# Performance work log

Hardware: AMD Instinct MI355X
Metric: run time of the kernel (lower is better)

## Reference

```python
import jax, jax.numpy as jnp
import numpy as np

B, R, H, W = 128, 8, 256, 256


def _conv(x, w, b):
    # x: [1, C_in, h, w], w: [C_out, C_in, 3, 3]; stride 2, pad 1, then bias + ReLU
    y = jax.lax.conv_general_dilated(
        x, w, window_strides=(2, 2), padding=((1, 1), (1, 1)),
        dimension_numbers=('NCHW', 'OIHW', 'NCHW'))
    return jax.nn.relu(y + b[None, :, None, None])


def _single(x, w1, b1, w2, b2, w3, b3, fw, fb):
    # x: [3, H, W]; one sample through its region's CNN expert
    h = x[None]                      # [1,3,H,W]
    h = _conv(h, w1, b1)             # [1,32,H/2,W/2]
    h = _conv(h, w2, b2)             # [1,64,H/4,W/4]
    h = _conv(h, w3, b3)             # [1,128,H/8,W/8]
    feat = h.mean(axis=(2, 3))[0]    # [128] global average pool
    return fw @ feat + fb            # [num_classes]


def setup_inputs() -> dict:
    key = jax.random.key(0)
    ks = jax.random.split(key, 10)
    s = 0.05
    return {
        'image': jax.random.normal(ks[0], (B, 3, H, W), jnp.float32),
        'region': jax.random.randint(ks[1], (B,), 0, R, jnp.int64),
        'w1': jax.random.normal(ks[2], (R, 32, 3, 3, 3), jnp.float32) * s,
        'b1': jax.random.normal(ks[3], (R, 32), jnp.float32) * s,
        'w2': jax.random.normal(ks[4], (R, 64, 32, 3, 3), jnp.float32) * s,
        'b2': jax.random.normal(ks[5], (R, 64), jnp.float32) * s,
        'w3': jax.random.normal(ks[6], (R, 128, 64, 3, 3), jnp.float32) * s,
        'b3': jax.random.normal(ks[7], (R, 128), jnp.float32) * s,
        'fw': jax.random.normal(ks[8], (R, 2, 128), jnp.float32) * s,
        'fb': jax.random.normal(ks[9], (R, 2), jnp.float32) * s,
    }


def reference(image, region, w1, b1, w2, b2, w3, b3, fw, fb):
    # MoE-style dispatch: gather each sample's region weights, vmap per-sample expert.
    r = region.astype(jnp.int32)
    pw = [jnp.take(p, r, axis=0) for p in (w1, b1, w2, b2, w3, b3, fw, fb)]
    out = jax.vmap(_single)(image, *pw)  # [B, num_classes]
    return out
```

## Files before the change

### kernel.cpp

```cpp
#include <hip/hip_runtime.h>
#include <cstdint>


typedef __attribute__((ext_vector_type(8))) short short8;
typedef __attribute__((ext_vector_type(4))) float floatx4;
typedef __attribute__((ext_vector_type(4))) unsigned short ushort4v;
typedef __attribute__((ext_vector_type(4))) float float4v;

__device__ inline unsigned short f2bf(float f) {
  union { float f; unsigned u; } x;
  x.f = f;
  unsigned u = x.u;
  u += 0x7FFFu + ((u >> 16) & 1u);
  return (unsigned short)(u >> 16);
}

__device__ inline void g2l16(const unsigned short* g, unsigned short* l) {
  __builtin_amdgcn_global_load_lds(
      (const __attribute__((address_space(1))) unsigned int*)g,
      (__attribute__((address_space(3))) unsigned int*)(unsigned int)(uintptr_t)l,
      16, 0, 0);
}

__global__ __launch_bounds__(256) void setup_k(
    const int* __restrict__ rp, int* __restrict__ rout, float* __restrict__ feat,
    const float* __restrict__ w1, unsigned short* __restrict__ w1p,
    const float* __restrict__ w2, unsigned short* __restrict__ w2p,
    const float* __restrict__ w3, unsigned short* __restrict__ w3p,
    unsigned short* __restrict__ h2p, int nhalo) {
  const int tid = threadIdx.x;
  if (blockIdx.x == 0) {
    __shared__ int is64;
    if (tid < 64) {
      int v = rp[2 * tid + 1];
      unsigned long long ball = __ballot(v != 0);
      if (tid == 0) is64 = (ball == 0ULL) ? 1 : 0;
    }
    __syncthreads();
    if (tid < 128) {
      int r = is64 ? rp[2 * tid] : rp[tid];
      rout[tid] = r & 7;
      float* fr = feat + tid * 128;
      for (int j = 0; j < 128; ++j) fr[j] = 0.f;
    }
    return;
  }
  int t = (blockIdx.x - 1) * 256 + tid;
  if (t < 16384) {
    int j = t & 7, lane = (t >> 3) & 63, mt = (t >> 9) & 1, kg = (t >> 10) & 1,
        r = t >> 11;
    int oc = mt * 16 + (lane & 15);
    int q = (lane >> 4) & 3;
    int row = kg * 2 + (q >> 1);
    int idx = (q & 1) * 8 + j;
    int kx = idx >> 2, c = idx & 3;
    float val = 0.f;
    if (row < 3 && kx < 3 && c < 3)
      val = w1[((r * 32 + oc) * 3 + c) * 9 + row * 3 + kx];
    w1p[t] = f2bf(val);
  } else if (t < 163840) {
    int t2 = t - 16384;
    int j = t2 & 7, lane = (t2 >> 3) & 63;
    int u = t2 >> 9;
    int mt = u & 3; u >>= 2;
    int tap = u % 9;
    int r = u / 9;
    int oc = mt * 16 + (lane & 15);
    int ic = ((lane >> 4) & 3) * 8 + j;
    w2p[t2] = f2bf(w2[((r * 64 + oc) * 32 + ic) * 9 + tap]);
  } else if (t < 753664) {
    int t3 = t - 163840;
    int j = t3 & 7, lane = (t3 >> 3) & 63;
    int u = t3 >> 9;
    int mt = u & 7; u >>= 3;
    int s = u & 1; u >>= 1;
    int tap = u % 9;
    int r = u / 9;
    int oc = mt * 16 + (lane & 15);
    int ic = s * 32 + ((lane >> 4) & 3) * 8 + j;
    w3p[t3] = f2bf(w3[((r * 128 + oc) * 64 + ic) * 9 + tap]);
  } else {
    int th = t - 753664;
    if (th < nhalo) {
      int s = th / 260, i = th - s * 260;
      int y, x;
      if (i < 66) { y = 0; x = i; }
      else if (i < 132) { y = 65; x = i - 66; }
      else {
        int ii = i - 132;
        y = 1 + (ii >> 1);
        x = (ii & 1) ? 65 : 0;
      }
      short8 z = {0, 0, 0, 0, 0, 0, 0, 0};
      *(short8*)(h2p + ((size_t)s * 66 * 66 + y * 66 + x) * 8) = z;
    }
  }
}

__global__ __launch_bounds__(256, 3) void conv12_k(
    const float* __restrict__ img, const unsigned short* __restrict__ w1p,
    const float* __restrict__ b1, const unsigned short* __restrict__ w2p,
    const float* __restrict__ b2, const int* __restrict__ rgn,
    unsigned short* __restrict__ outp, int b0) {
  __shared__ unsigned short imgT[11 * 168 * 4];
  __shared__ unsigned short h1T[9 * 4 * 66 * 8];
  __shared__ float sB1[32];
  __shared__ float sB2[64];
  const int tid = threadIdx.x;
  const int xh = blockIdx.x;
  const int oy0 = blockIdx.y * 4;
  const int bl = blockIdx.z;
  const int r = __builtin_amdgcn_readfirstlane(rgn[b0 + bl]);
  if (tid < 32) sB1[tid] = b1[r * 32 + tid];
  if (tid >= 64 && tid < 128) sB2[tid - 64] = b2[r * 64 + (tid - 64)];
  const float* ib = img + (size_t)(b0 + bl) * 3 * 65536;
  const int padx = xh ? 65 : 0;
  const bool skiptop = (oy0 == 0);
  const int rb = xh * 128 - 4;

  const int n = tid & 15, q = (tid >> 4) & 3, wv = tid >> 6;
  const int lane = tid & 63;
  const short8* wpb1 = (const short8*)w1p + (size_t)r * 256 + lane;
  short8 afr1[2][2];
#pragma unroll
  for (int kg = 0; kg < 2; ++kg)
#pragma unroll
    for (int m = 0; m < 2; ++m) afr1[kg][m] = wpb1[(kg * 2 + m) * 64];

  {
    const int nch = 11 * 41;
    for (int seg = 0; seg < nch; seg += 256) {
      int c = seg + tid;
      if (c < nch) {
        int i = c / 41, cq = c - i * 41;
        int rv = 4 * oy0 - 3 + i;
        int cb = rb + 4 * cq;
        unsigned short* dp = &imgT[((size_t)i * 168 + (4 * cq - 1)) * 4];
        if (rv >= 0 && cq > 0 && cb >= 0 && cb + 3 <= 255) {
          const float* p = ib + (size_t)rv * 256 + cb;
          float4v a = *(const float4v*)p;
          float4v bb = *(const float4v*)(p + 65536);
          float4v cc = *(const float4v*)(p + 131072);
#pragma unroll
          for (int e = 0; e < 4; ++e) {
            ushort4v v = {f2bf(a[e]), f2bf(bb[e]), f2bf(cc[e]), 0};
            *(ushort4v*)(dp + e * 4) = v;
          }
        } else {
          for (int e = (cq == 0 ? 1 : 0); e < 4; ++e) {
            int cc2 = cb + e;
            ushort4v v = {0, 0, 0, 0};
            if (rv >= 0 && cc2 >= 0 && cc2 <= 255) {
              const float* p = ib + (size_t)rv * 256 + cc2;
              v.x = f2bf(p[0]);
              v.y = f2bf(p[65536]);
              v.z = f2bf(p[131072]);
            }
            *(ushort4v*)(dp + e * 4) = v;
          }
        }
      }
    }
  }
  {
    short8 z8 = {0, 0, 0, 0, 0, 0, 0, 0};
    if (tid < 36) {
      int hy = tid / 4, cg = tid % 4;
      *(short8*)&h1T[(((size_t)hy * 4 + cg) * 66 + padx) * 8] = z8;
    }
    if (skiptop) {
      for (int c = tid; c < 264; c += 256) {
        int cg = c / 66, x = c - cg * 66;
        *(short8*)&h1T[(((size_t)0 * 4 + cg) * 66 + x) * 8] = z8;
      }
    }
  }

  auto CONV1ROW = [&](int hy, int phaseB) {
    floatx4 a1[5][2];
#pragma unroll
    for (int nt = 0; nt < 5; ++nt)
#pragma unroll
      for (int m = 0; m < 2; ++m) a1[nt][m] = (floatx4){0.f, 0.f, 0.f, 0.f};
#pragma unroll
    for (int kg = 0; kg < 2; ++kg) {
      int row = kg * 2 + (q >> 1);
      int rowc = (row < 3) ? row : 0;
      int tr = 2 * hy + rowc;
      int slot = phaseB ? (tr >= 11 ? tr - 11 : tr) : tr;
#pragma unroll
      for (int nt = 0; nt < 5; ++nt) {
        int lx = nt * 16 + n;
        short8 bfr = *(const short8*)&imgT[((size_t)slot * 168 + 2 * lx) * 4 +
                                           (q & 1) * 8];
#pragma unroll
        for (int m = 0; m < 2; ++m)
          a1[nt][m] = __builtin_amdgcn_mfma_f32_16x16x32_bf16(
              afr1[kg][m], bfr, a1[nt][m], 0, 0, 0);
      }
    }
#pragma unroll
    for (int nt = 0; nt < 5; ++nt) {
      int lx = nt * 16 + n;
      bool ok = (lx <= 65) && (lx != padx) && !(skiptop && hy == 0);
      if (ok) {
#pragma unroll
        for (int m = 0; m < 2; ++m) {
          ushort4v st;
#pragma unroll
          for (int rr = 0; rr < 4; ++rr) {
            float v = a1[nt][m][rr] + sB1[m * 16 + q * 4 + rr];
            st[rr] = f2bf(v > 0.f ? v : 0.f);
          }
          int cg = m * 2 + (q >> 1);
          *(ushort4v*)&h1T[(((size_t)hy * 4 + cg) * 66 + lx) * 8 +
                           (q & 1) * 4] = st;
        }
      }
    }
  };

  __syncthreads();

  float4v Lb0[3], Lb1[3];
  int ok0 = 0, ok1 = 0;
  {
    int c = tid;
    int i = c / 41, cq = c - i * 41;
    int cb = rb + 4 * cq;
    if (cq > 0 && cb >= 0 && cb + 3 <= 255) {
      const float* p = ib + (size_t)(4 * oy0 + 8 + i) * 256 + cb;
      Lb0[0] = *(const float4v*)p;
      Lb0[1] = *(const float4v*)(p + 65536);
      Lb0[2] = *(const float4v*)(p + 131072);
      ok0 = 1;
    }
    c = tid + 256;
    if (c < 328) {
      i = c / 41; cq = c - i * 41; cb = rb + 4 * cq;
      if (cq > 0 && cb >= 0 && cb + 3 <= 255) {
        const float* p = ib + (size_t)(4 * oy0 + 8 + i) * 256 + cb;
        Lb1[0] = *(const float4v*)p;
        Lb1[1] = *(const float4v*)(p + 65536);
        Lb1[2] = *(const float4v*)(p + 131072);
        ok1 = 1;
      }
    }
  }

  for (int hy = wv; hy <= 4; hy += 4) CONV1ROW(hy, 0);
  __syncthreads();

  auto STOREB = [&](int c, const float4v* L, int okf) {
    int i = c / 41, cq = c - i * 41;
    int cb = rb + 4 * cq;
    unsigned short* dp = &imgT[((size_t)i * 168 + (4 * cq - 1)) * 4];
    if (okf) {
#pragma unroll
      for (int e = 0; e < 4; ++e) {
        ushort4v v = {f2bf(L[0][e]), f2bf(L[1][e]), f2bf(L[2][e]), 0};
        *(ushort4v*)(dp + e * 4) = v;
      }
    } else {
      int rv = 4 * oy0 + 8 + i;
      for (int e = (cq == 0 ? 1 : 0); e < 4; ++e) {
        int cc2 = cb + e;
        ushort4v v = {0, 0, 0, 0};
        if (cc2 >= 0 && cc2 <= 255) {
          const float* p = ib + (size_t)rv * 256 + cc2;
          v.x = f2bf(p[0]);
          v.y = f2bf(p[65536]);
          v.z = f2bf(p[131072]);
        }
        *(ushort4v*)(dp + e * 4) = v;
      }
    }
  };
  STOREB(tid, Lb0, ok0);
  if (tid + 256 < 328) STOREB(tid + 256, Lb1, ok1);
  __syncthreads();

  CONV1ROW(5 + wv, 1);
  __syncthreads();

  const short8* wpb2 = (const short8*)w2p + (size_t)r * 9 * 4 * 64 + lane;
  floatx4 a2[2][4];
#pragma unroll
  for (int nt = 0; nt < 2; ++nt)
#pragma unroll
    for (int m = 0; m < 4; ++m) a2[nt][m] = (floatx4){0.f, 0.f, 0.f, 0.f};
#pragma unroll
  for (int tap = 0; tap < 9; ++tap) {
    const int ky = tap / 3, kx = tap % 3;
    short8 af[4];
#pragma unroll
    for (int m = 0; m < 4; ++m) af[m] = wpb2[(tap * 4 + m) * 64];
    short8 bf[2];
#pragma unroll
    for (int nt = 0; nt < 2; ++nt) {
      int ox = nt * 16 + n;
      bf[nt] = *(const short8*)&h1T[((((2 * wv + ky) << 2) + q) * 66 +
                                    (2 * ox + kx)) * 8];
    }
#pragma unroll
    for (int m = 0; m < 4; ++m)
#pragma unroll
      for (int nt = 0; nt < 2; ++nt)
        a2[nt][m] = __builtin_amdgcn_mfma_f32_16x16x32_bf16(af[m], bf[nt],
                                                            a2[nt][m], 0, 0, 0);
  }
  unsigned short* ob = outp + (size_t)bl * 8 * 66 * 66 * 8;
  const int oy = oy0 + wv;
#pragma unroll
  for (int nt = 0; nt < 2; ++nt) {
    int ox = xh * 32 + nt * 16 + n;
#pragma unroll
    for (int m = 0; m < 4; ++m) {
      ushort4v st;
#pragma unroll
      for (int rr = 0; rr < 4; ++rr) {
        float v = a2[nt][m][rr] + sB2[m * 16 + q * 4 + rr];
        st[rr] = f2bf(v > 0.f ? v : 0.f);
      }
      int cg = m * 2 + (q >> 1);
      *(ushort4v*)&ob[(((size_t)cg * 66 + oy + 1) * 66 + ox + 1) * 8 +
                      (q & 1) * 4] = st;
    }
  }
}

__global__ __launch_bounds__(256, 2) void conv3dir2_k(
    const unsigned short* __restrict__ in, const unsigned short* __restrict__ wp,
    const float* __restrict__ bias, const int* __restrict__ rgn,
    float* __restrict__ feat, int b0) {
  __shared__ float sBias[128];
  __shared__ float sGap[4 * 128];
  const int tid = threadIdx.x;
  const int bl = blockIdx.y;
  const int b = b0 + bl;
  const int r = __builtin_amdgcn_readfirstlane(rgn[b]);
  if (tid < 128) sBias[tid] = bias[r * 128 + tid];
  const int oyb = blockIdx.x * 8;
  const unsigned short* gbase = in + (size_t)bl * 8 * 66 * 66 * 8;
  const int lane = tid & 63, wv = tid >> 6;
  const int n = lane & 15, q = (lane >> 4) & 3;
  const short8* wpb = (const short8*)wp + (size_t)r * 9 * 2 * 8 * 64 + lane;

  floatx4 acc[2][2][8];
#pragma unroll
  for (int r2 = 0; r2 < 2; ++r2)
#pragma unroll
    for (int nt = 0; nt < 2; ++nt)
#pragma unroll
      for (int m = 0; m < 8; ++m) acc[r2][nt][m] = (floatx4){0.f, 0.f, 0.f, 0.f};

#pragma unroll
  for (int s = 0; s < 2; ++s) {
    const unsigned short* ab = gbase + (size_t)(s * 4 + q) * 66 * 66 * 8;
#pragma unroll
    for (int tap = 0; tap < 9; ++tap) {
      const int ky = tap / 3, kx = tap % 3;
      short8 bfr[2][2];
#pragma unroll
      for (int r2 = 0; r2 < 2; ++r2)
#pragma unroll
        for (int nt = 0; nt < 2; ++nt) {
          int oy = oyb + 2 * wv + r2;
          int ox = nt * 16 + n;
          bfr[r2][nt] = *(const short8*)&ab[((size_t)(2 * oy + ky) * 66 +
                                             (2 * ox + kx)) * 8];
        }
      short8 afr[8];
#pragma unroll
      for (int m = 0; m < 8; ++m) afr[m] = wpb[((tap * 2 + s) * 8 + m) * 64];
#pragma unroll
      for (int m = 0; m < 8; ++m)
#pragma unroll
        for (int r2 = 0; r2 < 2; ++r2)
#pragma unroll
          for (int nt = 0; nt < 2; ++nt)
            acc[r2][nt][m] = __builtin_amdgcn_mfma_f32_16x16x32_bf16(
                afr[m], bfr[r2][nt], acc[r2][nt][m], 0, 0, 0);
    }
  }

#pragma unroll
  for (int m = 0; m < 8; ++m)
#pragma unroll
    for (int rr = 0; rr < 4; ++rr) {
      float bv = sBias[m * 16 + q * 4 + rr];
      float vs = 0.f;
#pragma unroll
      for (int r2 = 0; r2 < 2; ++r2)
#pragma unroll
        for (int nt = 0; nt < 2; ++nt) {
          float v = acc[r2][nt][m][rr] + bv;
          vs += (v > 0.f ? v : 0.f);
        }
      vs += __shfl_xor(vs, 1, 16);
      vs += __shfl_xor(vs, 2, 16);
      vs += __shfl_xor(vs, 4, 16);
      vs += __shfl_xor(vs, 8, 16);
      if (n == 0) sGap[wv * 128 + m * 16 + q * 4 + rr] = vs;
    }
  __syncthreads();
  if (tid < 128)
    atomicAdd(&feat[b * 128 + tid],
              sGap[tid] + sGap[128 + tid] + sGap[256 + tid] + sGap[384 + tid]);
}

__global__ __launch_bounds__(256) void head_k(
    const float* __restrict__ feat, const float* __restrict__ fw,
    const float* __restrict__ fb, const int* __restrict__ rgn,
    float* __restrict__ out) {
  int t = threadIdx.x;
  int b = t >> 1, c = t & 1;
  int r = rgn[b];
  const float* fwr = fw + (r * 2 + c) * 128;
  const float* fv = feat + b * 128;
  float a = 0.f;
#pragma unroll 8
  for (int j = 0; j < 128; ++j) a = fmaf(fwr[j], fv[j], a);
  out[t] = a * (1.0f / 1024.0f) + fb[r * 2 + c];
}

extern "C" void kernel_launch(void* const* d_in, const int* in_sizes, int n_in,
                              void* d_out, int out_size, void* d_ws, size_t ws_size,
                              hipStream_t stream) {
  const float* img = (const float*)d_in[0];
  const int* rgn_raw = (const int*)d_in[1];
  const float* w1 = (const float*)d_in[2];
  const float* b1 = (const float*)d_in[3];
  const float* w2 = (const float*)d_in[4];
  const float* b2 = (const float*)d_in[5];
  const float* w3 = (const float*)d_in[6];
  const float* b3 = (const float*)d_in[7];
  const float* fw = (const float*)d_in[8];
  const float* fb = (const float*)d_in[9];
  float* out = (float*)d_out;

  const size_t h2p_s = (size_t)8 * 66 * 66 * 8 * 2;

  char* ws = (char*)d_ws;
  size_t off = 0;
  auto alloc = [&](size_t bytes) {
    char* p = ws + off;
    off += (bytes + 255) & ~(size_t)255;
    return p;
  };
  unsigned short* h2p = (unsigned short*)alloc((size_t)128 * h2p_s);
  unsigned short* w1p = (unsigned short*)alloc((size_t)16384 * 2);
  unsigned short* w2p = (unsigned short*)alloc((size_t)147456 * 2);
  unsigned short* w3p = (unsigned short*)alloc((size_t)589824 * 2);
  float* feat = (float*)alloc((size_t)128 * 128 * 4);
  int* rgn = (int*)alloc((size_t)128 * 4);

  {
    int nhalo = 128 * 8 * 260;
    int total = 753664 + nhalo;
    int nblk = 1 + (total + 255) / 256;
    hipLaunchKernelGGL(setup_k, dim3(nblk), dim3(256), 0, stream,
                       rgn_raw, rgn, feat, w1, w1p, w2, w2p, w3, w3p, h2p, nhalo);
  }

  hipLaunchKernelGGL(conv12_k, dim3(2, 16, 128), dim3(256), 0, stream,
                     img, w1p, b1, w2p, b2, rgn, h2p, 0);
  hipLaunchKernelGGL(conv3dir2_k, dim3(4, 128), dim3(256), 0, stream,
                     h2p, w3p, b3, rgn, feat, 0);
  hipLaunchKernelGGL(head_k, dim3(1), dim3(256), 0, stream, feat, fw, fb, rgn, out);
}
```

Measured before the change: 284.3 us.

## Halve conv1+conv2 row tile, drop two-phase image staging, vectorize head dot product

The fused conv1/conv2 kernel now produces 2 output rows per block instead of 4, so the grid doubles. The h1 LDS buffer shrinks, the occupancy hint rises from 3 to 4 blocks, and the second-phase image prefetch and register staging are removed. Each wave now computes one 16-pixel conv2 tile and loads weights per tap inside the loop. The price is more redundant conv1 halo rows and image reads per output row, and less weight reuse in registers. The head kernel's dot product is also vectorized with float4 loads and two accumulators.

Measured after the change: 298.2 us. +4.9%, slower.

```diff
diff --git a/kernel.cpp b/kernel.cpp
--- a/kernel.cpp
+++ b/kernel.cpp
@@ -13,13 +13,6 @@
   unsigned u = x.u;
   u += 0x7FFFu + ((u >> 16) & 1u);
   return (unsigned short)(u >> 16);
-}
-
-__device__ inline void g2l16(const unsigned short* g, unsigned short* l) {
-  __builtin_amdgcn_global_load_lds(
-      (const __attribute__((address_space(1))) unsigned int*)g,
-      (__attribute__((address_space(3))) unsigned int*)(unsigned int)(uintptr_t)l,
-      16, 0, 0);
 }
 
 __global__ __launch_bounds__(256) void setup_k(
@@ -97,18 +90,18 @@
   }
 }
 
-__global__ __launch_bounds__(256, 3) void conv12_k(
+__global__ __launch_bounds__(256, 4) void conv12b_k(
     const float* __restrict__ img, const unsigned short* __restrict__ w1p,
     const float* __restrict__ b1, const unsigned short* __restrict__ w2p,
     const float* __restrict__ b2, const int* __restrict__ rgn,
     unsigned short* __restrict__ outp, int b0) {
   __shared__ unsigned short imgT[11 * 168 * 4];
-  __shared__ unsigned short h1T[9 * 4 * 66 * 8];
+  __shared__ unsigned short h1T[5 * 4 * 66 * 8];
   __shared__ float sB1[32];
   __shared__ float sB2[64];
   const int tid = threadIdx.x;
   const int xh = blockIdx.x;
-  const int oy0 = blockIdx.y * 4;
+  const int oy0 = blockIdx.y * 2;
   const int bl = blockIdx.z;
   const int r = __builtin_amdgcn_readfirstlane(rgn[b0 + bl]);
   if (tid < 32) sB1[tid] = b1[r * 32 + tid];
@@ -164,8 +157,8 @@
   }
   {
     short8 z8 = {0, 0, 0, 0, 0, 0, 0, 0};
-    if (tid < 36) {
-      int hy = tid / 4, cg = tid % 4;
+    if (tid < 20) {
+      int hy = tid >> 2, cg = tid & 3;
       *(short8*)&h1T[(((size_t)hy * 4 + cg) * 66 + padx) * 8] = z8;
     }
     if (skiptop) {
@@ -175,8 +168,9 @@
       }
     }
   }
-
-  auto CONV1ROW = [&](int hy, int phaseB) {
+  __syncthreads();
+
+  auto CONV1ROW = [&](int hy) {
     floatx4 a1[5][2];
 #pragma unroll
     for (int nt = 0; nt < 5; ++nt)
@@ -187,11 +181,10 @@
       int row = kg * 2 + (q >> 1);
       int rowc = (row < 3) ? row : 0;
       int tr = 2 * hy + rowc;
-      int slot = phaseB ? (tr >= 11 ? tr - 11 : tr) : tr;
 #pragma unroll
       for (int nt = 0; nt < 5; ++nt) {
         int lx = nt * 16 + n;
-        short8 bfr = *(const short8*)&imgT[((size_t)slot * 168 + 2 * lx) * 4 +
+        short8 bfr = *(const short8*)&imgT[((size_t)tr * 168 + 2 * lx) * 4 +
                                            (q & 1) * 8];
 #pragma unroll
         for (int m = 0; m < 2; ++m)
@@ -219,113 +212,41 @@
       }
     }
   };
-
+  CONV1ROW(wv);
+  if (wv == 0) CONV1ROW(4);
   __syncthreads();
 
-  float4v Lb0[3], Lb1[3];
-  int ok0 = 0, ok1 = 0;
-  {
-    int c = tid;
-    int i = c / 41, cq = c - i * 41;
-    int cb = rb + 4 * cq;
-    if (cq > 0 && cb >= 0 && cb + 3 <= 255) {
-      const float* p = ib + (size_t)(4 * oy0 + 8 + i) * 256 + cb;
-      Lb0[0] = *(const float4v*)p;
-      Lb0[1] = *(const float4v*)(p + 65536);
-      Lb0[2] = *(const float4v*)(p + 131072);
-      ok0 = 1;
-    }
-    c = tid + 256;
-    if (c < 328) {
-      i = c / 41; cq = c - i * 41; cb = rb + 4 * cq;
-      if (cq > 0 && cb >= 0 && cb + 3 <= 255) {
-        const float* p = ib + (size_t)(4 * oy0 + 8 + i) * 256 + cb;
-        Lb1[0] = *(const float4v*)p;
-        Lb1[1] = *(const float4v*)(p + 65536);
-        Lb1[2] = *(const float4v*)(p + 131072);
-        ok1 = 1;
-      }
-    }
-  }
-
-  for (int hy = wv; hy <= 4; hy += 4) CONV1ROW(hy, 0);
-  __syncthreads();
-
-  auto STOREB = [&](int c, const float4v* L, int okf) {
-    int i = c / 41, cq = c - i * 41;
-    int cb = rb + 4 * cq;
-    unsigned short* dp = &imgT[((size_t)i * 168 + (4 * cq - 1)) * 4];
-    if (okf) {
-#pragma unroll
-      for (int e = 0; e < 4; ++e) {
-        ushort4v v = {f2bf(L[0][e]), f2bf(L[1][e]), f2bf(L[2][e]), 0};
-        *(ushort4v*)(dp + e * 4) = v;
-      }
-    } else {
-      int rv = 4 * oy0 + 8 + i;
-      for (int e = (cq == 0 ? 1 : 0); e < 4; ++e) {
-        int cc2 = cb + e;
-        ushort4v v = {0, 0, 0, 0};
-        if (cc2 >= 0 && cc2 <= 255) {
-          const float* p = ib + (size_t)rv * 256 + cc2;
-          v.x = f2bf(p[0]);
-          v.y = f2bf(p[65536]);
-          v.z = f2bf(p[131072]);
-        }
-        *(ushort4v*)(dp + e * 4) = v;
-      }
-    }
-  };
-  STOREB(tid, Lb0, ok0);
-  if (tid + 256 < 328) STOREB(tid + 256, Lb1, ok1);
-  __syncthreads();
-
-  CONV1ROW(5 + wv, 1);
-  __syncthreads();
-
+  const int c2r = wv >> 1, c2h = wv & 1;
   const short8* wpb2 = (const short8*)w2p + (size_t)r * 9 * 4 * 64 + lane;
-  floatx4 a2[2][4];
-#pragma unroll
-  for (int nt = 0; nt < 2; ++nt)
-#pragma unroll
-    for (int m = 0; m < 4; ++m) a2[nt][m] = (floatx4){0.f, 0.f, 0.f, 0.f};
+  floatx4 a2[4];
+#pragma unroll
+  for (int m = 0; m < 4; ++m) a2[m] = (floatx4){0.f, 0.f, 0.f, 0.f};
 #pragma unroll
   for (int tap = 0; tap < 9; ++tap) {
     const int ky = tap / 3, kx = tap % 3;
-    short8 af[4];
-#pragma unroll
-    for (int m = 0; m < 4; ++m) af[m] = wpb2[(tap * 4 + m) * 64];
-    short8 bf[2];
-#pragma unroll
-    for (int nt = 0; nt < 2; ++nt) {
-      int ox = nt * 16 + n;
-      bf[nt] = *(const short8*)&h1T[((((2 * wv + ky) << 2) + q) * 66 +
-                                    (2 * ox + kx)) * 8];
-    }
-#pragma unroll
-    for (int m = 0; m < 4; ++m)
-#pragma unroll
-      for (int nt = 0; nt < 2; ++nt)
-        a2[nt][m] = __builtin_amdgcn_mfma_f32_16x16x32_bf16(af[m], bf[nt],
-                                                            a2[nt][m], 0, 0, 0);
+    const int oxl = c2h * 16 + n;
+    short8 bf = *(const short8*)&h1T[((((2 * c2r + ky) << 2) + q) * 66 +
+                                     (2 * oxl + kx)) * 8];
+#pragma unroll
+    for (int m = 0; m < 4; ++m) {
+      short8 af = wpb2[(tap * 4 + m) * 64];
+      a2[m] = __builtin_amdgcn_mfma_f32_16x16x32_bf16(af, bf, a2[m], 0, 0, 0);
+    }
   }
   unsigned short* ob = outp + (size_t)bl * 8 * 66 * 66 * 8;
-  const int oy = oy0 + wv;
-#pragma unroll
-  for (int nt = 0; nt < 2; ++nt) {
-    int ox = xh * 32 + nt * 16 + n;
-#pragma unroll
-    for (int m = 0; m < 4; ++m) {
-      ushort4v st;
-#pragma unroll
-      for (int rr = 0; rr < 4; ++rr) {
-        float v = a2[nt][m][rr] + sB2[m * 16 + q * 4 + rr];
-        st[rr] = f2bf(v > 0.f ? v : 0.f);
-      }
-      int cg = m * 2 + (q >> 1);
-      *(ushort4v*)&ob[(((size_t)cg * 66 + oy + 1) * 66 + ox + 1) * 8 +
-                      (q & 1) * 4] = st;
-    }
+  const int oy = oy0 + c2r;
+  const int ox = xh * 32 + c2h * 16 + n;
+#pragma unroll
+  for (int m = 0; m < 4; ++m) {
+    ushort4v st;
+#pragma unroll
+    for (int rr = 0; rr < 4; ++rr) {
+      float v = a2[m][rr] + sB2[m * 16 + q * 4 + rr];
+      st[rr] = f2bf(v > 0.f ? v : 0.f);
+    }
+    int cg = m * 2 + (q >> 1);
+    *(ushort4v*)&ob[(((size_t)cg * 66 + oy + 1) * 66 + ox + 1) * 8 +
+                    (q & 1) * 4] = st;
   }
 }
 
@@ -416,11 +337,16 @@
   int t = threadIdx.x;
   int b = t >> 1, c = t & 1;
   int r = rgn[b];
-  const float* fwr = fw + (r * 2 + c) * 128;
-  const float* fv = feat + b * 128;
-  float a = 0.f;
-#pragma unroll 8
-  for (int j = 0; j < 128; ++j) a = fmaf(fwr[j], fv[j], a);
+  const float4v* fwr = (const float4v*)(fw + (r * 2 + c) * 128);
+  const float4v* fv = (const float4v*)(feat + b * 128);
+  float4v s0 = {0.f, 0.f, 0.f, 0.f}, s1 = {0.f, 0.f, 0.f, 0.f};
+#pragma unroll
+  for (int j = 0; j < 32; j += 2) {
+    s0 += fwr[j] * fv[j];
+    s1 += fwr[j + 1] * fv[j + 1];
+  }
+  float4v s = s0 + s1;
+  float a = (s[0] + s[1]) + (s[2] + s[3]);
   out[t] = a * (1.0f / 1024.0f) + fb[r * 2 + c];
 }
 
@@ -463,7 +389,7 @@
                        rgn_raw, rgn, feat, w1, w1p, w2, w2p, w3, w3p, h2p, nhalo);
   }
 
-  hipLaunchKernelGGL(conv12_k, dim3(2, 16, 128), dim3(256), 0, stream,
+  hipLaunchKernelGGL(conv12b_k, dim3(2, 32, 128), dim3(256), 0, stream,
                      img, w1p, b1, w2p, b2, rgn, h2p, 0);
   hipLaunchKernelGGL(conv3dir2_k, dim3(4, 128), dim3(256), 0, stream,
                      h2p, w3p, b3, rgn, feat, 0);
```
